# Kernel optimization log

Hardware: AMD Instinct MI355X
Metric: run time of the kernel (lower is better)

## Reference

```python
import jax, jax.numpy as jnp
import numpy as np

N_KNOTS = 10
NC = 32
BATCH = 32
EPS = 1e-5

def _spline_matrix(n):
    step = 1.0 / (n - 1.0)
    mat = 4 * np.eye(n - 2)
    np.fill_diagonal(mat[1:, :-1], 1)
    np.fill_diagonal(mat[:-1, 1:], 1)
    A = 6 * np.linalg.inv(mat) / step ** 2
    z = np.zeros(n - 2)
    A = np.vstack([z, A, z])            # [n, n-2]
    B = np.zeros((n - 2, n))
    np.fill_diagonal(B, 1)
    np.fill_diagonal(B[:, 1:], -2)
    np.fill_diagonal(B[:, 2:], 1)
    return np.dot(A, B).astype(np.float32)  # [n, n]

def setup_inputs() -> dict:
    key = jax.random.key(0)
    ks = jax.random.split(key, 8)
    n, nc = N_KNOTS, NC
    inp = {}
    inp['batch'] = jax.random.uniform(ks[0], (BATCH, 3, 256, 256), dtype=jnp.float32)
    chans = [3, nc, 2 * nc, 4 * nc, 8 * nc, 16 * nc]
    for i in range(5):
        ci, co = chans[i], chans[i + 1]
        inp['c%d_w' % (i + 1)] = jax.random.normal(jax.random.fold_in(ks[1], i), (co, ci, 3, 3), dtype=jnp.float32) * 0.1
        inp['c%d_b' % (i + 1)] = jnp.zeros((co,), jnp.float32)
        inp['bn%d_g' % (i + 1)] = jnp.ones((co,), jnp.float32)
        inp['bn%d_b' % (i + 1)] = jnp.zeros((co,), jnp.float32)
    inp['l1_w'] = jax.random.normal(ks[2], (100 * n, 16 * nc * 7 * 7), dtype=jnp.float32) * 0.02
    inp['l1_b'] = jnp.zeros((100 * n,), jnp.float32)
    inp['l2_w'] = jax.random.normal(ks[3], (3 * n, 100 * n), dtype=jnp.float32) * 0.02
    inp['l2_b'] = jnp.zeros((3 * n,), jnp.float32)
    inp['matrix'] = jnp.asarray(_spline_matrix(n))
    return inp

def _conv_bn(x, w, b, g, be):
    # conv (stride 2, VALID) -> relu -> batchnorm (training-mode batch stats)
    y = jax.lax.conv_general_dilated(x, w, (2, 2), 'VALID', dimension_numbers=('NCHW', 'OIHW', 'NCHW'))
    y = jax.nn.relu(y + b[None, :, None, None])
    m = jnp.mean(y, axis=(0, 2, 3))
    v = jnp.var(y, axis=(0, 2, 3))
    inv = jax.lax.rsqrt(v + EPS)
    return g[None, :, None, None] * (y - m[None, :, None, None]) * inv[None, :, None, None] + be[None, :, None, None]

def _forward(batch, c1_w, c1_b, bn1_g, bn1_b, c2_w, c2_b, bn2_g, bn2_b,
             c3_w, c3_b, bn3_g, bn3_b, c4_w, c4_b, bn4_g, bn4_b,
             c5_w, c5_b, bn5_g, bn5_b, l1_w, l1_b, l2_w, l2_b, matrix):
    n = matrix.shape[0]
    h = 1.0 / (n - 1.0)  # knot spacing (self.step)
    B, _, H, W = batch.shape

    x = _conv_bn(batch, c1_w, c1_b, bn1_g, bn1_b)
    x = _conv_bn(x, c2_w, c2_b, bn2_g, bn2_b)
    x = _conv_bn(x, c3_w, c3_b, bn3_g, bn3_b)
    x = _conv_bn(x, c4_w, c4_b, bn4_g, bn4_b)
    x = _conv_bn(x, c5_w, c5_b, bn5_g, bn5_b)
    x = x.reshape(B, -1)
    x = jax.nn.relu(x @ l1_w.T + l1_b)
    x = x @ l2_w.T + l2_b
    ys = x.reshape(B, 3, n) / 100.0

    identity = jnp.arange(n, dtype=batch.dtype) / (n - 1)
    ys_aug = ys + identity                                    # [B,3,n]
    # second-derivative values M at knots (natural cubic spline solve as dense matmul)
    M = jnp.einsum('ij,bcj->bci', matrix, ys_aug)             # [B,3,n]
    a = (M[..., 1:] - M[..., :-1]) / (6 * h)                  # [B,3,n-1]
    b_ = M[..., :-1] / 2
    c_ = (ys_aug[..., 1:] - ys_aug[..., :-1]) / h - (M[..., 1:] + 2 * M[..., :-1]) * (h / 6)
    d_ = ys_aug[..., :-1]

    def eval_spline(xv):  # xv: [B,3,K] -> [B,3,K]; gather segment coeffs instead of one-hot matmul
        xi = jnp.clip(jnp.floor(xv / h), 0, n - 2).astype(jnp.int32)
        xf = xv - xi.astype(xv.dtype) * h
        ag = jnp.take_along_axis(a, xi, axis=-1)
        bg = jnp.take_along_axis(b_, xi, axis=-1)
        cg = jnp.take_along_axis(c_, xi, axis=-1)
        dg = jnp.take_along_axis(d_, xi, axis=-1)
        return ((ag * xf + bg) * xf + cg) * xf + dg

    out = eval_spline(batch.reshape(B, 3, H * W)).reshape(B, 3, H, W)
    vals = jnp.arange(255, dtype=batch.dtype) / 255.0          # arange(0,1,1/255)
    splines = eval_spline(jnp.broadcast_to(vals, (B, 3, 255)))
    return out, splines

def reference(batch, c1_w, c1_b, bn1_g, bn1_b, c2_w, c2_b, bn2_g, bn2_b,
              c3_w, c3_b, bn3_g, bn3_b, c4_w, c4_b, bn4_g, bn4_b,
              c5_w, c5_b, bn5_g, bn5_b, l1_w, l1_b, l2_w, l2_b, matrix):
    return _forward(batch, c1_w, c1_b, bn1_g, bn1_b, c2_w, c2_b, bn2_g, bn2_b,
                    c3_w, c3_b, bn3_g, bn3_b, c4_w, c4_b, bn4_g, bn4_b,
                    c5_w, c5_b, bn5_g, bn5_b, l1_w, l1_b, l2_w, l2_b, matrix)
```

## Files before the change

### kernel.cpp

```cpp
#include <hip/hip_runtime.h>
#include <hip/hip_bf16.h>

#define BEPS 1e-5f
#define FC1_KS 98
#define FC1_KC 256
#define C1NB 2017
#define STS 512

typedef __attribute__((ext_vector_type(8))) short short8v;
typedef __attribute__((ext_vector_type(4))) float f32x4;
typedef unsigned short ushort_t;

__device__ __forceinline__ float bf2f(ushort_t u) {
    unsigned int x = ((unsigned int)u) << 16;
    return __builtin_bit_cast(float, x);
}
__device__ __forceinline__ ushort_t f2bf(float v) {
    __hip_bfloat16 h = __float2bfloat16(v);
    return *(ushort_t*)&h;
}

__global__ __launch_bounds__(256) void conv1_direct(
    const float* __restrict__ in, const float* __restrict__ w,
    const float* __restrict__ bias, ushort_t* __restrict__ out) {
    __shared__ float ws[864];
    __shared__ float bs[32];
    const int tid = threadIdx.x;
    for (int i = tid; i < 864; i += 256) ws[i] = w[i];
    if (tid < 32) bs[tid] = bias[tid];
    __syncthreads();

    const int TOT = 32 * 16129;
    int p = blockIdx.x * 256 + tid;
    if (p >= TOT) return;
    int b = p / 16129, pp = p - b * 16129;
    int i = pp / 127, j = pp - i * 127;
    const float* ib = in + ((long long)b * 3) * 65536 + (2 * i) * 256 + 2 * j;
    float patch[27];
#pragma unroll
    for (int ci = 0; ci < 3; ++ci)
#pragma unroll
        for (int di = 0; di < 3; ++di) {
            const float* rp = ib + ci * 65536 + di * 256;
            float2 v01 = *(const float2*)rp;
            patch[ci * 9 + di * 3 + 0] = v01.x;
            patch[ci * 9 + di * 3 + 1] = v01.y;
            patch[ci * 9 + di * 3 + 2] = rp[2];
        }

    ushort_t res[32];
#pragma unroll
    for (int co = 0; co < 32; co += 4) {
        float a0 = bs[co], a1 = bs[co + 1], a2 = bs[co + 2], a3 = bs[co + 3];
#pragma unroll
        for (int t = 0; t < 27; ++t) {
            float pv = patch[t];
            a0 = fmaf(pv, ws[(co + 0) * 27 + t], a0);
            a1 = fmaf(pv, ws[(co + 1) * 27 + t], a1);
            a2 = fmaf(pv, ws[(co + 2) * 27 + t], a2);
            a3 = fmaf(pv, ws[(co + 3) * 27 + t], a3);
        }
        res[co + 0] = f2bf(fmaxf(a0, 0.f));
        res[co + 1] = f2bf(fmaxf(a1, 0.f));
        res[co + 2] = f2bf(fmaxf(a2, 0.f));
        res[co + 3] = f2bf(fmaxf(a3, 0.f));
    }
    ushort_t* ob = out + (long long)p * 32;
#pragma unroll
    for (int v = 0; v < 4; ++v)
        *(short8v*)&ob[v * 8] = *(const short8v*)&res[v * 8];
}

__global__ __launch_bounds__(256) void conv_mfma(
    const ushort_t* __restrict__ in, const ushort_t* __restrict__ wf,
    const float* __restrict__ effb, ushort_t* __restrict__ out,
    float* __restrict__ pacc,
    int B, int Ci, int lgCi, int Hi, int Wi, int Co, int Ho, int Wo,
    int K, int Kp, int kcount) {
    const int HoWo = Ho * Wo;
    const int N = B * HoWo;
    __shared__ __align__(16) ushort_t As[64 * 64];
    __shared__ __align__(16) ushort_t Bs[128 * 64];
    const int tid = threadIdx.x;
    const int m0 = blockIdx.y * 64;
    const int n0 = blockIdx.x * 128;
    const int kbeg = blockIdx.z * kcount;

    const int rowA = tid >> 2;
    const int kqA = (tid & 3) * 16;
    const ushort_t* wrowA = wf + (long long)(m0 + rowA) * Kp + kbeg + kqA;
    const int swA = (rowA & 7) << 3;
    const int rowB = tid >> 1;
    const int kqB = (tid & 1) * 32;
    const int n = n0 + rowB;
    const int nn = (n < N) ? n : (N - 1);
    const int pb = nn / HoWo, pp = nn - pb * HoWo;
    const int pi = pp / Wo, pj = pp - pi * Wo;
    const long long base0 = ((long long)pb * Hi + 2 * pi) * Wi + 2 * pj;
    const int swB = (rowB & 7) << 3;

    const int w = tid >> 6;
    const int lane = tid & 63;
    const int wco = (w >> 1) * 32, wpx = (w & 1) * 64;
    const int lm = lane & 15, lk = lane >> 4;

    f32x4 acc[2][4] = {};
    for (int k0 = 0; k0 < kcount; k0 += 64) {
        {
            short8v a0 = *(const short8v*)(wrowA + k0);
            short8v a1 = *(const short8v*)(wrowA + k0 + 8);
            *(short8v*)&As[rowA * 64 + ((kqA + 0) ^ swA)] = a0;
            *(short8v*)&As[rowA * 64 + ((kqA + 8) ^ swA)] = a1;
        }
#pragma unroll
        for (int ch = 0; ch < 2; ++ch) {
            int c16 = kqB + ch * 16;
            int kg = kbeg + k0 + c16;
            int tap = kg >> lgCi;
            tap = tap > 8 ? 8 : tap;
            int ci0 = kg & (Ci - 1);
            int dy = tap / 3, dx = tap - dy * 3;
            const ushort_t* src = in + (base0 + dy * Wi + dx) * Ci + ci0;
            short8v v0 = *(const short8v*)src;
            short8v v1 = *(const short8v*)(src + 8);
            *(short8v*)&Bs[rowB * 64 + ((c16 + 0) ^ swB)] = v0;
            *(short8v*)&Bs[rowB * 64 + ((c16 + 8) ^ swB)] = v1;
        }
        __syncthreads();
#pragma unroll
        for (int kk = 0; kk < 2; ++kk) {
            const int kb = kk * 32 + lk * 8;
            const int ra0 = wco + lm, ra1 = wco + 16 + lm;
            short8v a0 = *(const short8v*)&As[ra0 * 64 + (kb ^ ((ra0 & 7) << 3))];
            short8v a1 = *(const short8v*)&As[ra1 * 64 + (kb ^ ((ra1 & 7) << 3))];
            const int rb0 = wpx + lm, rb1 = wpx + 16 + lm;
            const int rb2 = wpx + 32 + lm, rb3 = wpx + 48 + lm;
            short8v b0 = *(const short8v*)&Bs[rb0 * 64 + (kb ^ ((rb0 & 7) << 3))];
            short8v b1 = *(const short8v*)&Bs[rb1 * 64 + (kb ^ ((rb1 & 7) << 3))];
            short8v b2 = *(const short8v*)&Bs[rb2 * 64 + (kb ^ ((rb2 & 7) << 3))];
            short8v b3 = *(const short8v*)&Bs[rb3 * 64 + (kb ^ ((rb3 & 7) << 3))];
            acc[0][0] = __builtin_amdgcn_mfma_f32_16x16x32_bf16(a0, b0, acc[0][0], 0, 0, 0);
            acc[0][1] = __builtin_amdgcn_mfma_f32_16x16x32_bf16(a0, b1, acc[0][1], 0, 0, 0);
            acc[0][2] = __builtin_amdgcn_mfma_f32_16x16x32_bf16(a0, b2, acc[0][2], 0, 0, 0);
            acc[0][3] = __builtin_amdgcn_mfma_f32_16x16x32_bf16(a0, b3, acc[0][3], 0, 0, 0);
            acc[1][0] = __builtin_amdgcn_mfma_f32_16x16x32_bf16(a1, b0, acc[1][0], 0, 0, 0);
            acc[1][1] = __builtin_amdgcn_mfma_f32_16x16x32_bf16(a1, b1, acc[1][1], 0, 0, 0);
            acc[1][2] = __builtin_amdgcn_mfma_f32_16x16x32_bf16(a1, b2, acc[1][2], 0, 0, 0);
            acc[1][3] = __builtin_amdgcn_mfma_f32_16x16x32_bf16(a1, b3, acc[1][3], 0, 0, 0);
        }
        __syncthreads();
    }
    if (pacc) {
        float* pbuf = pacc + ((long long)blockIdx.z * N) * Co;
#pragma unroll
        for (int nb = 0; nb < 4; ++nb) {
            int np = n0 + wpx + nb * 16 + lm;
            if (np >= N) continue;
#pragma unroll
            for (int amr = 0; amr < 2; ++amr) {
                int cobase = m0 + wco + amr * 16 + lk * 4;
                float4 vv = make_float4(acc[amr][nb][0], acc[amr][nb][1],
                                        acc[amr][nb][2], acc[amr][nb][3]);
                *(float4*)&pbuf[(long long)np * Co + cobase] = vv;
            }
        }
    } else {
#pragma unroll
        for (int nb = 0; nb < 4; ++nb) {
            int np = n0 + wpx + nb * 16 + lm;
            if (np >= N) continue;
#pragma unroll
            for (int amr = 0; amr < 2; ++amr) {
                int cobase = m0 + wco + amr * 16 + lk * 4;
                float4 eb = *(const float4*)&effb[cobase];
                ushort4 u;
                u.x = f2bf(fmaxf(acc[amr][nb][0] + eb.x, 0.f));
                u.y = f2bf(fmaxf(acc[amr][nb][1] + eb.y, 0.f));
                u.z = f2bf(fmaxf(acc[amr][nb][2] + eb.z, 0.f));
                u.w = f2bf(fmaxf(acc[amr][nb][3] + eb.w, 0.f));
                *(ushort4*)&out[(long long)np * Co + cobase] = u;
            }
        }
    }
}

__global__ void convz_reduce(const float* __restrict__ pacc, const float* __restrict__ effb,
                             ushort_t* __restrict__ out, int N, int Co, int lgCo, int Z,
                             int total) {
    int idx = blockIdx.x * 256 + threadIdx.x;
    if (idx >= total) return;
    int c = idx & (Co - 1);
    float s = effb[c];
    for (int z = 0; z < Z; ++z) s += pacc[((long long)z * N << lgCo) + idx];
    out[idx] = f2bf(fmaxf(s, 0.f));
}

__global__ __launch_bounds__(256) void stats_flat(
    const ushort_t* __restrict__ y, float* __restrict__ part,
    long long total, int C, int S) {
    const int tid = threadIdx.x;
    float sum[8] = {}, sq[8] = {};
    const long long nchunk = (total + 2047) >> 11;
    for (long long g = blockIdx.x; g < nchunk; g += S) {
        long long off = (g << 11) + tid * 8;
        if (off + 8 <= total) {
            short8v v8 = *(const short8v*)(y + off);
#pragma unroll
            for (int j = 0; j < 8; ++j) {
                float v = bf2f((ushort_t)v8[j]);
                sum[j] += v;
                sq[j] = fmaf(v, v, sq[j]);
            }
        }
    }
    __shared__ float rs[256][8], rq[256][8];
#pragma unroll
    for (int j = 0; j < 8; ++j) { rs[tid][j] = sum[j]; rq[tid][j] = sq[j]; }
    __syncthreads();
    const int G = C >> 3;
    const int TPG = 256 / G;
    for (int c = tid; c < C; c += 256) {
        int grp = c >> 3, j = c & 7;
        float s = 0.f, q = 0.f;
        for (int i = 0; i < TPG; ++i) {
            s += rs[grp + i * G][j];
            q += rq[grp + i * G][j];
        }
        part[(c * S + blockIdx.x) * 2 + 0] = s;
        part[(c * S + blockIdx.x) * 2 + 1] = q;
    }
}

__global__ __launch_bounds__(256) void stats_final_w(
    const float* __restrict__ part, const float* __restrict__ g,
    const float* __restrict__ be, float* __restrict__ scale,
    float* __restrict__ shift, int C, int S, float invN) {
    int c = blockIdx.x * 4 + (threadIdx.x >> 6);
    int lane = threadIdx.x & 63;
    if (c >= C) return;
    float s = 0.f, q = 0.f;
    for (int i = lane; i < S; i += 64) {
        s += part[(c * S + i) * 2 + 0];
        q += part[(c * S + i) * 2 + 1];
    }
#pragma unroll
    for (int off = 32; off > 0; off >>= 1) {
        s += __shfl_down(s, off, 64);
        q += __shfl_down(q, off, 64);
    }
    if (lane == 0) {
        float m = s * invN;
        float v = q * invN - m * m;
        float inv = rsqrtf(v + BEPS);
        float sc = g[c] * inv;
        scale[c] = sc;
        shift[c] = be[c] - m * sc;
    }
}

__global__ void fold_w_nhwc(const float* __restrict__ w, const float* __restrict__ scale,
                            ushort_t* __restrict__ wout, int Ci, int lgCi, int K, int Kp) {
    int k = blockIdx.x * 256 + threadIdx.x;
    int co = blockIdx.y;
    if (k >= Kp) return;
    ushort_t o = 0;
    if (k < K) {
        int tap = k >> lgCi;
        int ci = k & (Ci - 1);
        o = f2bf(w[((long long)co * Ci + ci) * 9 + tap] * scale[ci]);
    }
    wout[(long long)co * Kp + k] = o;
}

__global__ __launch_bounds__(256) void fold_b_v2(
    const float* __restrict__ w, const float* __restrict__ shift,
    const float* __restrict__ bias, float* __restrict__ effb, int Co, int Ci) {
    const int co = blockIdx.x * 4 + (threadIdx.x >> 6);
    const int lane = threadIdx.x & 63;
    if (co >= Co) return;
    const int CK = Ci * 9;
    const float* wr = w + (long long)co * CK;
    float acc = 0.f;
    for (int k = lane; k < CK; k += 64) acc = fmaf(wr[k], shift[k / 9], acc);
#pragma unroll
    for (int off = 32; off > 0; off >>= 1) acc += __shfl_down(acc, off, 64);
    if (lane == 0) effb[co] = acc + bias[co];
}

__global__ void bn_apply_t(const ushort_t* __restrict__ y, const float* __restrict__ scale,
                           const float* __restrict__ shift, float* __restrict__ xT) {
    int idx = blockIdx.x * blockDim.x + threadIdx.x;
    if (idx >= 802816) return;
    int k = idx >> 5, b = idx & 31;
    int c = k / 49, p = k - c * 49;
    float v = bf2f(y[((long long)b * 49 + p) * 512 + c]);
    xT[idx] = fmaf(v, scale[c], shift[c]);
}

__global__ __launch_bounds__(256) void fc1_gemm(const float* __restrict__ xT,
                                                const float* __restrict__ w,
                                                float* __restrict__ part) {
    const int K = 25088;
    __shared__ __align__(16) float As[16][64];
    __shared__ __align__(16) float Bs[16][32];
    const int tid = threadIdx.x;
    const int m0 = blockIdx.y * 64;
    const int kbeg = blockIdx.x * FC1_KC;
    const int cA = tid >> 2;
    const int kqA = (tid & 3) * 4;
    const int kkB = tid >> 5;
    const int bB = tid & 31;
    const int tm = tid >> 4;
    const int tn = tid & 15;

    const int mrow = m0 + cA;
    const bool mvalid = (mrow < 1000);
    const float* wrow = w + (long long)mrow * K + kbeg + kqA;

    float acc[4][2] = {};
    for (int k0 = 0; k0 < FC1_KC; k0 += 16) {
        float4 av = mvalid ? *(const float4*)(wrow + k0)
                           : make_float4(0.f, 0.f, 0.f, 0.f);
        As[kqA + 0][cA] = av.x;
        As[kqA + 1][cA] = av.y;
        As[kqA + 2][cA] = av.z;
        As[kqA + 3][cA] = av.w;
#pragma unroll
        for (int e = 0; e < 2; ++e) {
            int kk = kkB + e * 8;
            Bs[kk][bB] = xT[(kbeg + k0 + kk) * 32 + bB];
        }
        __syncthreads();
#pragma unroll
        for (int kk = 0; kk < 16; ++kk) {
            float4 a = *(const float4*)&As[kk][tm * 4];
            float b0 = Bs[kk][tn * 2 + 0];
            float b1 = Bs[kk][tn * 2 + 1];
            float a4[4] = {a.x, a.y, a.z, a.w};
#pragma unroll
            for (int mi = 0; mi < 4; ++mi) {
                acc[mi][0] = fmaf(a4[mi], b0, acc[mi][0]);
                acc[mi][1] = fmaf(a4[mi], b1, acc[mi][1]);
            }
        }
        __syncthreads();
    }
    float* pb = part + ((long long)blockIdx.y * FC1_KS + blockIdx.x) * 2048;
#pragma unroll
    for (int mi = 0; mi < 4; ++mi) {
        pb[(tm * 4 + mi) * 32 + tn * 2 + 0] = acc[mi][0];
        pb[(tm * 4 + mi) * 32 + tn * 2 + 1] = acc[mi][1];
    }
}

__global__ void fc1_reduce(const float* __restrict__ part, const float* __restrict__ bias,
                           float* __restrict__ z) {
    int idx = blockIdx.x * blockDim.x + threadIdx.x;
    if (idx >= 32000) return;
    int o = idx >> 5, b = idx & 31;
    int mt = o >> 6, mr = o & 63;
    const float* p = part + ((long long)mt * FC1_KS) * 2048 + mr * 32 + b;
    float s0 = 0.f, s1 = 0.f;
    int ks = 0;
    for (; ks + 1 < FC1_KS; ks += 2) {
        s0 += p[(long long)ks * 2048];
        s1 += p[(long long)(ks + 1) * 2048];
    }
    for (; ks < FC1_KS; ++ks) s0 += p[(long long)ks * 2048];
    z[b * 1000 + o] = fmaxf(s0 + s1 + bias[o], 0.f);
}

__global__ __launch_bounds__(256) void fc2_v2(const float* __restrict__ z,
                                              const float* __restrict__ w,
                                              const float* __restrict__ bias,
                                              float* __restrict__ ys) {
    int gid = blockIdx.x * 4 + (threadIdx.x >> 6);
    int lane = threadIdx.x & 63;
    if (gid >= 960) return;
    int b = gid / 30, o = gid - b * 30;
    const float* zr = z + (long long)b * 1000;
    const float* wr = w + (long long)o * 1000;
    float acc = 0.f;
    for (int k = lane; k < 1000; k += 64) acc = fmaf(zr[k], wr[k], acc);
    for (int off = 32; off > 0; off >>= 1) acc += __shfl_down(acc, off, 64);
    if (lane == 0) ys[gid] = acc + bias[o];
}

__global__ void spline_coeff(const float* __restrict__ ysraw, const float* __restrict__ matrix,
                             float4* __restrict__ coef) {
    int r = threadIdx.x;
    if (r >= 96) return;
    const float h = 1.0f / 9.0f;
    float ya[10];
    int b = r / 3, ch = r % 3;
#pragma unroll
    for (int j = 0; j < 10; ++j)
        ya[j] = ysraw[b * 30 + ch * 10 + j] / 100.0f + (float)j / 9.0f;
    float M[10];
#pragma unroll
    for (int i = 0; i < 10; ++i) {
        float acc = 0.f;
#pragma unroll
        for (int j = 0; j < 10; ++j) acc = fmaf(matrix[i * 10 + j], ya[j], acc);
        M[i] = acc;
    }
#pragma unroll
    for (int k = 0; k < 9; ++k) {
        float a = (M[k + 1] - M[k]) / (6.0f * h);
        float bb = M[k] * 0.5f;
        float cc = (ya[k + 1] - ya[k]) / h - (M[k + 1] + 2.0f * M[k]) * (h / 6.0f);
        float dd = ya[k];
        coef[r * 9 + k] = make_float4(a, bb, cc, dd);
    }
}

__global__ void eval_img4(const float4* __restrict__ batch4, const float4* __restrict__ coef,
                          float4* __restrict__ out4) {
    int idx = blockIdx.x * blockDim.x + threadIdx.x;
    if (idx >= 1572864) return;
    int plane = idx >> 14;
    float4 xv4 = batch4[idx];
    const float h = 1.0f / 9.0f;
    float xin[4] = {xv4.x, xv4.y, xv4.z, xv4.w};
    float xout[4];
#pragma unroll
    for (int e = 0; e < 4; ++e) {
        float xv = xin[e];
        int xi = (int)floorf(xv / h);
        xi = min(max(xi, 0), 8);
        float xf = xv - (float)xi * h;
        float4 cf = coef[plane * 9 + xi];
        xout[e] = fmaf(fmaf(fmaf(cf.x, xf, cf.y), xf, cf.z), xf, cf.w);
    }
    out4[idx] = make_float4(xout[0], xout[1], xout[2], xout[3]);
}

__global__ void eval_tab(const float4* __restrict__ coef, float* __restrict__ out, int total) {
    int idx = blockIdx.x * blockDim.x + threadIdx.x;
    if (idx >= total) return;
    int plane = idx / 255;
    int j = idx % 255;
    float xv = (float)j / 255.0f;
    const float h = 1.0f / 9.0f;
    int xi = (int)floorf(xv / h);
    xi = min(max(xi, 0), 8);
    float xf = xv - (float)xi * h;
    float4 cf = coef[plane * 9 + xi];
    out[idx] = fmaf(fmaf(fmaf(cf.x, xf, cf.y), xf, cf.z), xf, cf.w);
}

extern "C" void kernel_launch(void* const* d_in, const int* in_sizes, int n_in,
                              void* d_out, int out_size, void* d_ws, size_t ws_size,
                              hipStream_t stream) {
    const int B = 32;
    const float* batch = (const float*)d_in[0];
    const float* cw[5] = {(const float*)d_in[1], (const float*)d_in[5], (const float*)d_in[9],
                          (const float*)d_in[13], (const float*)d_in[17]};
    const float* cb[5] = {(const float*)d_in[2], (const float*)d_in[6], (const float*)d_in[10],
                          (const float*)d_in[14], (const float*)d_in[18]};
    const float* bg[5] = {(const float*)d_in[3], (const float*)d_in[7], (const float*)d_in[11],
                          (const float*)d_in[15], (const float*)d_in[19]};
    const float* bb[5] = {(const float*)d_in[4], (const float*)d_in[8], (const float*)d_in[12],
                          (const float*)d_in[16], (const float*)d_in[20]};
    const float* l1w = (const float*)d_in[21];
    const float* l1b = (const float*)d_in[22];
    const float* l2w = (const float*)d_in[23];
    const float* l2b = (const float*)d_in[24];
    const float* matrix = (const float*)d_in[25];

    float* f = (float*)d_ws;
    const size_t A_F = 8258048;
    const size_t Bq_F = 4064256;
    const size_t W_F = 589824;
    ushort_t* bufA = (ushort_t*)f;
    ushort_t* bufB = (ushort_t*)(f + A_F);
    ushort_t* Wf_bf = (ushort_t*)(f + A_F + Bq_F);
    float* effb  = f + A_F + Bq_F + W_F;
    float* scale = effb + 512;
    float* shift = scale + 512;
    float* part  = shift + 512;
    float* x5    = part + 524288;
    float* pacc  = x5 + 802816;
    float* z1    = pacc + 3686400;
    float* ysb   = z1 + 32000;
    float4* coef = (float4*)(ysb + 960);

    const int Ci[5]   = {3, 32, 64, 128, 256};
    const int lgCi[5] = {0, 5, 6, 7, 8};
    const int Co[5]   = {32, 64, 128, 256, 512};
    const int Hi[5]   = {256, 127, 63, 31, 15};
    const int Ho[5]   = {127, 63, 31, 15, 7};
    const int Zl[5]   = {1, 1, 1, 2, 3};

    ushort_t* bufs[2] = {bufA, bufB};

    conv1_direct<<<C1NB, 256, 0, stream>>>(batch, cw[0], cb[0], bufA);
    {
        long long total = (long long)B * 16129 * 32;
        stats_flat<<<STS, 256, 0, stream>>>(bufA, part, total, 32, STS);
        stats_final_w<<<8, 256, 0, stream>>>(part, bg[0], bb[0], scale, shift, 32, STS,
                                             32.0f / (float)total);
    }

    const ushort_t* cur = bufA;
    for (int l = 1; l < 5; ++l) {
        ushort_t* outb = bufs[l % 2];
        int K = Ci[l] * 9;
        int Kp = (K + 63) & ~63;
        fold_w_nhwc<<<dim3((Kp + 255) / 256, Co[l]), 256, 0, stream>>>(
            cw[l], scale, Wf_bf, Ci[l], lgCi[l], K, Kp);
        fold_b_v2<<<(Co[l] + 3) / 4, 256, 0, stream>>>(cw[l], shift, cb[l], effb, Co[l], Ci[l]);
        int N = B * Ho[l] * Ho[l];
        int Z = Zl[l];
        int kcount = Kp / Z;
        dim3 grid((N + 127) / 128, Co[l] / 64, Z);
        if (Z == 1) {
            conv_mfma<<<grid, 256, 0, stream>>>(cur, Wf_bf, effb, outb, nullptr,
                                                B, Ci[l], lgCi[l], Hi[l], Hi[l], Co[l],
                                                Ho[l], Ho[l], K, Kp, kcount);
        } else {
            conv_mfma<<<grid, 256, 0, stream>>>(cur, Wf_bf, effb, nullptr, pacc,
                                                B, Ci[l], lgCi[l], Hi[l], Hi[l], Co[l],
                                                Ho[l], Ho[l], K, Kp, kcount);
            int total = N * Co[l];
            int lgCo = (Co[l] == 256) ? 8 : 9;
            convz_reduce<<<(total + 255) / 256, 256, 0, stream>>>(pacc, effb, outb,
                                                                  N, Co[l], lgCo, Z, total);
        }
        long long total = (long long)N * Co[l];
        stats_flat<<<STS, 256, 0, stream>>>(outb, part, total, Co[l], STS);
        stats_final_w<<<(Co[l] + 3) / 4, 256, 0, stream>>>(part, bg[l], bb[l], scale, shift,
                                                           Co[l], STS, (float)Co[l] / (float)total);
        cur = outb;
    }

    bn_apply_t<<<(802816 + 255) / 256, 256, 0, stream>>>(cur, scale, shift, x5);
    {
        dim3 grid(FC1_KS, 16);
        fc1_gemm<<<grid, 256, 0, stream>>>(x5, l1w, pacc);
    }
    fc1_reduce<<<(32000 + 255) / 256, 256, 0, stream>>>(pacc, l1b, z1);
    fc2_v2<<<240, 256, 0, stream>>>(z1, l2w, l2b, ysb);
    spline_coeff<<<1, 96, 0, stream>>>(ysb, matrix, coef);

    float* out = (float*)d_out;
    eval_img4<<<(1572864 + 255) / 256, 256, 0, stream>>>((const float4*)batch, coef,
                                                         (float4*)out);
    eval_tab<<<(96 * 255 + 255) / 256, 256, 0, stream>>>(coef, out + 6291456, 96 * 255);
}
```

Baseline: 287.2 us.

## Use bf16 MFMA for FC1 and merge fold and spline-eval kernels

Replaces the scalar fp32 FC1 GEMM with a bf16 MFMA kernel that converts the fp32 weights to bf16 on load into swizzled shared memory. The BN-apply step now writes bf16 activations in batch-major layout to feed it. It also fuses the weight-fold and bias-fold kernels into one launch and merges the two spline evaluation kernels, cutting launch count. Dropping FC1 inputs to bf16 trades precision for compute throughput.

```diff
diff --git a/kernel.cpp b/kernel.cpp
--- a/kernel.cpp
+++ b/kernel.cpp
@@ -258,98 +258,110 @@
     }
 }
 
-__global__ void fold_w_nhwc(const float* __restrict__ w, const float* __restrict__ scale,
-                            ushort_t* __restrict__ wout, int Ci, int lgCi, int K, int Kp) {
-    int k = blockIdx.x * 256 + threadIdx.x;
-    int co = blockIdx.y;
-    if (k >= Kp) return;
-    ushort_t o = 0;
-    if (k < K) {
-        int tap = k >> lgCi;
-        int ci = k & (Ci - 1);
-        o = f2bf(w[((long long)co * Ci + ci) * 9 + tap] * scale[ci]);
-    }
-    wout[(long long)co * Kp + k] = o;
-}
-
-__global__ __launch_bounds__(256) void fold_b_v2(
-    const float* __restrict__ w, const float* __restrict__ shift,
-    const float* __restrict__ bias, float* __restrict__ effb, int Co, int Ci) {
-    const int co = blockIdx.x * 4 + (threadIdx.x >> 6);
-    const int lane = threadIdx.x & 63;
-    if (co >= Co) return;
-    const int CK = Ci * 9;
-    const float* wr = w + (long long)co * CK;
-    float acc = 0.f;
-    for (int k = lane; k < CK; k += 64) acc = fmaf(wr[k], shift[k / 9], acc);
-#pragma unroll
-    for (int off = 32; off > 0; off >>= 1) acc += __shfl_down(acc, off, 64);
-    if (lane == 0) effb[co] = acc + bias[co];
-}
-
-__global__ void bn_apply_t(const ushort_t* __restrict__ y, const float* __restrict__ scale,
-                           const float* __restrict__ shift, float* __restrict__ xT) {
+__global__ __launch_bounds__(256) void fold_fused(
+    const float* __restrict__ w, const float* __restrict__ scale,
+    const float* __restrict__ shift, const float* __restrict__ bias,
+    ushort_t* __restrict__ wout, float* __restrict__ effb,
+    int Ci, int lgCi, int K, int Kp, int Co, int WB) {
+    if ((int)blockIdx.x < WB) {
+        int idx = blockIdx.x * 256 + threadIdx.x;
+        if (idx >= Co * Kp) return;
+        int co = idx / Kp, k = idx - co * Kp;
+        ushort_t o = 0;
+        if (k < K) {
+            int tap = k >> lgCi;
+            int ci = k & (Ci - 1);
+            o = f2bf(w[((long long)co * Ci + ci) * 9 + tap] * scale[ci]);
+        }
+        wout[idx] = o;
+    } else {
+        int co = ((int)blockIdx.x - WB) * 4 + (threadIdx.x >> 6);
+        int lane = threadIdx.x & 63;
+        if (co >= Co) return;
+        const int CK = Ci * 9;
+        const float* wr = w + (long long)co * CK;
+        float acc = 0.f;
+        for (int k = lane; k < CK; k += 64) acc = fmaf(wr[k], shift[k / 9], acc);
+#pragma unroll
+        for (int off = 32; off > 0; off >>= 1) acc += __shfl_down(acc, off, 64);
+        if (lane == 0) effb[co] = acc + bias[co];
+    }
+}
+
+__global__ void bn_apply_x(const ushort_t* __restrict__ y, const float* __restrict__ scale,
+                           const float* __restrict__ shift, ushort_t* __restrict__ xB) {
     int idx = blockIdx.x * blockDim.x + threadIdx.x;
     if (idx >= 802816) return;
-    int k = idx >> 5, b = idx & 31;
+    int b = idx / 25088, k = idx - b * 25088;
     int c = k / 49, p = k - c * 49;
     float v = bf2f(y[((long long)b * 49 + p) * 512 + c]);
-    xT[idx] = fmaf(v, scale[c], shift[c]);
-}
-
-__global__ __launch_bounds__(256) void fc1_gemm(const float* __restrict__ xT,
-                                                const float* __restrict__ w,
-                                                float* __restrict__ part) {
+    xB[idx] = f2bf(fmaf(v, scale[c], shift[c]));
+}
+
+__global__ __launch_bounds__(256) void fc1_mfma(
+    const float* __restrict__ w, const ushort_t* __restrict__ xB,
+    float* __restrict__ part) {
     const int K = 25088;
-    __shared__ __align__(16) float As[16][64];
-    __shared__ __align__(16) float Bs[16][32];
+    __shared__ __align__(16) ushort_t As[64 * 256];
+    __shared__ __align__(16) ushort_t Bs[32 * 256];
     const int tid = threadIdx.x;
     const int m0 = blockIdx.y * 64;
     const int kbeg = blockIdx.x * FC1_KC;
-    const int cA = tid >> 2;
-    const int kqA = (tid & 3) * 4;
-    const int kkB = tid >> 5;
-    const int bB = tid & 31;
-    const int tm = tid >> 4;
-    const int tn = tid & 15;
-
-    const int mrow = m0 + cA;
-    const bool mvalid = (mrow < 1000);
-    const float* wrow = w + (long long)mrow * K + kbeg + kqA;
-
-    float acc[4][2] = {};
-    for (int k0 = 0; k0 < FC1_KC; k0 += 16) {
-        float4 av = mvalid ? *(const float4*)(wrow + k0)
-                           : make_float4(0.f, 0.f, 0.f, 0.f);
-        As[kqA + 0][cA] = av.x;
-        As[kqA + 1][cA] = av.y;
-        As[kqA + 2][cA] = av.z;
-        As[kqA + 3][cA] = av.w;
-#pragma unroll
-        for (int e = 0; e < 2; ++e) {
-            int kk = kkB + e * 8;
-            Bs[kk][bB] = xT[(kbeg + k0 + kk) * 32 + bB];
-        }
-        __syncthreads();
-#pragma unroll
-        for (int kk = 0; kk < 16; ++kk) {
-            float4 a = *(const float4*)&As[kk][tm * 4];
-            float b0 = Bs[kk][tn * 2 + 0];
-            float b1 = Bs[kk][tn * 2 + 1];
-            float a4[4] = {a.x, a.y, a.z, a.w};
-#pragma unroll
-            for (int mi = 0; mi < 4; ++mi) {
-                acc[mi][0] = fmaf(a4[mi], b0, acc[mi][0]);
-                acc[mi][1] = fmaf(a4[mi], b1, acc[mi][1]);
+
+    {
+        const int r = tid >> 2;
+        const int kq = (tid & 3) * 64;
+        const int m = m0 + r;
+        const bool mv = (m < 1000);
+        const float* wr = w + (long long)m * K + kbeg + kq;
+        const int sw = (r & 7) << 3;
+#pragma unroll
+        for (int g = 0; g < 8; ++g) {
+            short8v o = {0, 0, 0, 0, 0, 0, 0, 0};
+            if (mv) {
+                float4 f0 = *(const float4*)(wr + g * 8);
+                float4 f1 = *(const float4*)(wr + g * 8 + 4);
+                o[0] = (short)f2bf(f0.x); o[1] = (short)f2bf(f0.y);
+                o[2] = (short)f2bf(f0.z); o[3] = (short)f2bf(f0.w);
+                o[4] = (short)f2bf(f1.x); o[5] = (short)f2bf(f1.y);
+                o[6] = (short)f2bf(f1.z); o[7] = (short)f2bf(f1.w);
             }
-        }
-        __syncthreads();
+            *(short8v*)&As[r * 256 + ((kq + g * 8) ^ sw)] = o;
+        }
+    }
+    {
+        const int b = tid >> 3;
+        const int kq = (tid & 7) * 32;
+        const ushort_t* xr = xB + (long long)b * K + kbeg + kq;
+        const int sw = (b & 7) << 3;
+#pragma unroll
+        for (int g = 0; g < 4; ++g) {
+            short8v v = *(const short8v*)(xr + g * 8);
+            *(short8v*)&Bs[b * 256 + ((kq + g * 8) ^ sw)] = v;
+        }
+    }
+    __syncthreads();
+    const int wv = tid >> 6, lane = tid & 63;
+    const int lm = lane & 15, lk = lane >> 4;
+    const int wm = wv * 16;
+    f32x4 acc0 = {}, acc1 = {};
+    const int ra = wm + lm;
+    const int swa = (ra & 7) << 3;
+    const int swb = (lm & 7) << 3;
+#pragma unroll
+    for (int s = 0; s < 8; ++s) {
+        int kb = s * 32 + lk * 8;
+        short8v av = *(const short8v*)&As[ra * 256 + (kb ^ swa)];
+        short8v b0 = *(const short8v*)&Bs[lm * 256 + (kb ^ swb)];
+        short8v b1 = *(const short8v*)&Bs[(16 + lm) * 256 + (kb ^ swb)];
+        acc0 = __builtin_amdgcn_mfma_f32_16x16x32_bf16(av, b0, acc0, 0, 0, 0);
+        acc1 = __builtin_amdgcn_mfma_f32_16x16x32_bf16(av, b1, acc1, 0, 0, 0);
     }
     float* pb = part + ((long long)blockIdx.y * FC1_KS + blockIdx.x) * 2048;
 #pragma unroll
-    for (int mi = 0; mi < 4; ++mi) {
-        pb[(tm * 4 + mi) * 32 + tn * 2 + 0] = acc[mi][0];
-        pb[(tm * 4 + mi) * 32 + tn * 2 + 1] = acc[mi][1];
+    for (int r = 0; r < 4; ++r) {
+        pb[(wm + lk * 4 + r) * 32 + lm] = acc0[r];
+        pb[(wm + lk * 4 + r) * 32 + 16 + lm] = acc1[r];
     }
 }
 
@@ -414,39 +426,37 @@
     }
 }
 
-__global__ void eval_img4(const float4* __restrict__ batch4, const float4* __restrict__ coef,
-                          float4* __restrict__ out4) {
+__global__ void eval_all(const float4* __restrict__ batch4, const float4* __restrict__ coef,
+                         float4* __restrict__ out4, float* __restrict__ outt) {
     int idx = blockIdx.x * blockDim.x + threadIdx.x;
-    if (idx >= 1572864) return;
-    int plane = idx >> 14;
-    float4 xv4 = batch4[idx];
     const float h = 1.0f / 9.0f;
-    float xin[4] = {xv4.x, xv4.y, xv4.z, xv4.w};
-    float xout[4];
-#pragma unroll
-    for (int e = 0; e < 4; ++e) {
-        float xv = xin[e];
+    if (idx < 1572864) {
+        int plane = idx >> 14;
+        float4 xv4 = batch4[idx];
+        float xin[4] = {xv4.x, xv4.y, xv4.z, xv4.w};
+        float xout[4];
+#pragma unroll
+        for (int e = 0; e < 4; ++e) {
+            float xv = xin[e];
+            int xi = (int)floorf(xv / h);
+            xi = min(max(xi, 0), 8);
+            float xf = xv - (float)xi * h;
+            float4 cf = coef[plane * 9 + xi];
+            xout[e] = fmaf(fmaf(fmaf(cf.x, xf, cf.y), xf, cf.z), xf, cf.w);
+        }
+        out4[idx] = make_float4(xout[0], xout[1], xout[2], xout[3]);
+    } else {
+        int t = idx - 1572864;
+        if (t >= 96 * 255) return;
+        int plane = t / 255;
+        int j = t - plane * 255;
+        float xv = (float)j / 255.0f;
         int xi = (int)floorf(xv / h);
         xi = min(max(xi, 0), 8);
         float xf = xv - (float)xi * h;
         float4 cf = coef[plane * 9 + xi];
-        xout[e] = fmaf(fmaf(fmaf(cf.x, xf, cf.y), xf, cf.z), xf, cf.w);
-    }
-    out4[idx] = make_float4(xout[0], xout[1], xout[2], xout[3]);
-}
-
-__global__ void eval_tab(const float4* __restrict__ coef, float* __restrict__ out, int total) {
-    int idx = blockIdx.x * blockDim.x + threadIdx.x;
-    if (idx >= total) return;
-    int plane = idx / 255;
-    int j = idx % 255;
-    float xv = (float)j / 255.0f;
-    const float h = 1.0f / 9.0f;
-    int xi = (int)floorf(xv / h);
-    xi = min(max(xi, 0), 8);
-    float xf = xv - (float)xi * h;
-    float4 cf = coef[plane * 9 + xi];
-    out[idx] = fmaf(fmaf(fmaf(cf.x, xf, cf.y), xf, cf.z), xf, cf.w);
+        outt[t] = fmaf(fmaf(fmaf(cf.x, xf, cf.y), xf, cf.z), xf, cf.w);
+    }
 }
 
 extern "C" void kernel_launch(void* const* d_in, const int* in_sizes, int n_in,
@@ -507,9 +517,10 @@
         ushort_t* outb = bufs[l % 2];
         int K = Ci[l] * 9;
         int Kp = (K + 63) & ~63;
-        fold_w_nhwc<<<dim3((Kp + 255) / 256, Co[l]), 256, 0, stream>>>(
-            cw[l], scale, Wf_bf, Ci[l], lgCi[l], K, Kp);
-        fold_b_v2<<<(Co[l] + 3) / 4, 256, 0, stream>>>(cw[l], shift, cb[l], effb, Co[l], Ci[l]);
+        int WB = (Co[l] * Kp + 255) / 256;
+        int BBk = (Co[l] + 3) / 4;
+        fold_fused<<<WB + BBk, 256, 0, stream>>>(cw[l], scale, shift, cb[l], Wf_bf, effb,
+                                                 Ci[l], lgCi[l], K, Kp, Co[l], WB);
         int N = B * Ho[l] * Ho[l];
         int Z = Zl[l];
         int kcount = Kp / Z;
@@ -534,17 +545,18 @@
         cur = outb;
     }
 
-    bn_apply_t<<<(802816 + 255) / 256, 256, 0, stream>>>(cur, scale, shift, x5);
+    ushort_t* xB = (ushort_t*)x5;
+    bn_apply_x<<<(802816 + 255) / 256, 256, 0, stream>>>(cur, scale, shift, xB);
     {
         dim3 grid(FC1_KS, 16);
-        fc1_gemm<<<grid, 256, 0, stream>>>(x5, l1w, pacc);
+        fc1_mfma<<<grid, 256, 0, stream>>>(l1w, xB, pacc);
     }
     fc1_reduce<<<(32000 + 255) / 256, 256, 0, stream>>>(pacc, l1b, z1);
     fc2_v2<<<240, 256, 0, stream>>>(z1, l2w, l2b, ysb);
     spline_coeff<<<1, 96, 0, stream>>>(ysb, matrix, coef);
 
     float* out = (float*)d_out;
-    eval_img4<<<(1572864 + 255) / 256, 256, 0, stream>>>((const float4*)batch, coef,
-                                                         (float4*)out);
-    eval_tab<<<(96 * 255 + 255) / 256, 256, 0, stream>>>(coef, out + 6291456, 96 * 255);
-}
+    int evtot = 1572864 + 96 * 255;
+    eval_all<<<(evtot + 255) / 256, 256, 0, stream>>>((const float4*)batch, coef,
+                                                      (float4*)out, out + 6291456);
+}
```

Measured after the change: 258.7 us. -9.9%, faster.
